# Kernel tuning notes

Hardware: AMD Instinct MI355X
Metric: run time of the kernel (lower is better)

Reference implementation:

```python
import jax, jax.numpy as jnp
import numpy as np

N, E, CIN, A, C, NB, B = 20000, 100000, 64, 32, 256, 4, 128
FD = C * NB  # fusion_dims = channels + c_growth*(n_blocks_out-1) with c_growth==channels
HID = 1024


def setup_inputs() -> dict:
    key = jax.random.key(0)
    ks = jax.random.split(key, 24)
    s = 0.05
    inp = {
        "x": jax.random.normal(ks[0], (N, CIN), jnp.float32),
        "edges": jax.random.randint(ks[1], (2, E), 0, N, jnp.int32),
        "edge_weights": jax.random.uniform(ks[2], (E,), jnp.float32),
        "edge_attrs": jax.random.normal(ks[3], (E, A), jnp.float32),
        "bbox_idx": jax.random.randint(ks[4], (N,), 0, B, jnp.int32),
        "num_boxes": B,
        # head GraphConv params: message MLP on [x_dst, x_src-x_dst, edge_attr]
        "W_msg0": jax.random.normal(ks[5], (2 * CIN + A, C), jnp.float32) * s,
        "b_msg0": jnp.zeros((C,), jnp.float32),
        "W_sup0": jax.random.normal(ks[6], (C + CIN, C), jnp.float32) * s,
        "b_sup0": jnp.zeros((C,), jnp.float32),
        # ResBlock params (n_blocks-1 blocks)
        "W_msg": jax.random.normal(ks[7], (NB - 1, 2 * C + A, C), jnp.float32) * s,
        "b_msg": jnp.zeros((NB - 1, C), jnp.float32),
        "W_sup": jax.random.normal(ks[8], (NB - 1, 2 * C, C), jnp.float32) * s,
        "b_sup": jnp.zeros((NB - 1, C), jnp.float32),
        # fusion MLPs [fusion_dims -> 1024]
        "W_fuse": jax.random.normal(ks[9], (FD, HID), jnp.float32) * s,
        "b_fuse": jnp.zeros((HID,), jnp.float32),
        "W_fuse_sup": jax.random.normal(ks[10], (FD, HID), jnp.float32) * s,
        "b_fuse_sup": jnp.zeros((HID,), jnp.float32),
    }
    return inp


def reference(x, edge_weights, edge_attrs, W_msg0, b_msg0, W_sup0, b_sup0,
              W_msg, b_msg, W_sup, b_sup, W_fuse, b_fuse, W_fuse_sup, b_fuse_sup,
              edges, bbox_idx, num_boxes):
    src, dst = edges[0], edges[1]
    n = x.shape[0]

    def gconv(f_in, Wm, bm):
        # per-edge message on [f_dst, f_src - f_dst, edge_attr], weighted sum-aggregate to dst
        h = jnp.concatenate([f_in[dst], f_in[src] - f_in[dst], edge_attrs], axis=1)
        m = jax.nn.relu(h @ Wm + bm) * edge_weights[:, None]
        return jax.ops.segment_sum(m, dst, num_segments=n)

    def super_node(f, x_node, Ws, bs):
        return jax.nn.relu(jnp.concatenate([f, x_node], axis=1) @ Ws + bs)

    # head GraphConv
    f = gconv(x, W_msg0, b_msg0)
    fs = super_node(f, x, W_sup0, b_sup0)
    feats, feats_super = [f], [fs]
    # ResBlocks: residual on node features, fresh super features
    for i in range(NB - 1):
        f = gconv(feats[-1], W_msg[i], b_msg[i]) + feats[-1]
        fs = super_node(f, feats_super[-1], W_sup[i], b_sup[i])
        feats.append(f)
        feats_super.append(fs)

    # n_blocks_out == n_blocks -> take all blocks
    feats_cat = jnp.concatenate(feats, axis=1)            # [N, FD]
    fusion = jax.nn.relu(feats_cat @ W_fuse + b_fuse)     # [N, 1024]
    out_feat = jnp.concatenate([fusion, feats_cat], axis=1)

    fs_cat = jnp.concatenate(feats_super, axis=1)         # [N, FD]
    sums = jax.ops.segment_sum(fs_cat, bbox_idx, num_segments=num_boxes)
    cnts = jax.ops.segment_sum(jnp.ones((n, 1), fs_cat.dtype), bbox_idx, num_segments=num_boxes)
    fs_mean = sums / jnp.maximum(cnts, 1.0)               # scatter(reduce='mean')
    fusion_sup = jax.nn.relu(fs_mean @ W_fuse_sup + b_fuse_sup)
    out_feat_super = jnp.concatenate([fusion_sup, fs_mean], axis=1)
    return out_feat, out_feat_super
```

## Files before the change

### kernel.cpp

```cpp
#include <hip/hip_runtime.h>

#define N_NODES 20000
#define N_EDGES 100000
#define CIN     64
#define A_DIM   32
#define CCH     256
#define NBOX    128
#define FD      1024
#define HID     1024
#define OUT_STRIDE 2048

typedef __attribute__((ext_vector_type(8))) short          short8;
typedef __attribute__((ext_vector_type(8))) unsigned short ushort8;
typedef __attribute__((ext_vector_type(4))) unsigned short ushort4v;
typedef __attribute__((ext_vector_type(4))) float          floatx4;

__device__ __forceinline__ unsigned short f2bf(float f) {
    unsigned int u = __float_as_uint(f);
    u += 0x7fff + ((u >> 16) & 1);
    return (unsigned short)(u >> 16);
}
__device__ __forceinline__ float bf2f(unsigned short h) {
    return __uint_as_float(((unsigned int)h) << 16);
}

__device__ __forceinline__ void glds16(const unsigned short* g, unsigned short* l) {
    __builtin_amdgcn_global_load_lds(
        (const __attribute__((address_space(1))) unsigned int*)g,
        (__attribute__((address_space(3))) unsigned int*)l,
        16, 0, 0);
}

struct GD {
    const unsigned short* src0b;
    const unsigned short* src1b;
    const unsigned short* Wt;
    const float* bias;
    const int* ridx0;
    float* outf;
    unsigned short* outb;
    int s0, o0, C0, s1, o1, do_relu, sof, oof, sob, oob, rmode, M, K, nbc;
};

__global__ __launch_bounds__(256) void mfma_dense(GD A, GD B, int n0)
{
    __shared__ __align__(16) unsigned short SM[2][4096];

    const int tid = threadIdx.x;
    const bool fa = (int)blockIdx.x < n0;

    const unsigned short* src0b = fa ? A.src0b : B.src0b;
    const unsigned short* src1b = fa ? A.src1b : B.src1b;
    const unsigned short* Wt    = fa ? A.Wt    : B.Wt;
    const float* bias           = fa ? A.bias  : B.bias;
    const int*   ridx0          = fa ? A.ridx0 : B.ridx0;
    float* outf                 = fa ? A.outf  : B.outf;
    unsigned short* outb        = fa ? A.outb  : B.outb;
    const int s0  = fa ? A.s0  : B.s0,  o0  = fa ? A.o0  : B.o0;
    const int C0  = fa ? A.C0  : B.C0;
    const int s1  = fa ? A.s1  : B.s1,  o1  = fa ? A.o1  : B.o1;
    const int do_relu = fa ? A.do_relu : B.do_relu;
    const int sof = fa ? A.sof : B.sof, oof = fa ? A.oof : B.oof;
    const int sob = fa ? A.sob : B.sob, oob = fa ? A.oob : B.oob;
    const int rmode = fa ? A.rmode : B.rmode;
    const int M   = fa ? A.M   : B.M;
    const int K   = fa ? A.K   : B.K;
    const int nbc = fa ? A.nbc : B.nbc;

    const int nwg = fa ? n0 : (int)gridDim.x - n0;
    const int lb  = (int)blockIdx.x - (fa ? 0 : n0);
    const int q8  = nwg >> 3, r8 = nwg & 7;
    const int xcd = lb & 7, boff = lb >> 3;
    const int bid = (xcd < r8 ? xcd * (q8 + 1)
                              : r8 * (q8 + 1) + (xcd - r8) * q8) + boff;

    const int rb   = bid / nbc, cb = bid % nbc;
    const int r0   = rb * 128, c0 = cb * 128;
    const int wave = tid >> 6, lane = tid & 63;
    const int quad = lane >> 4, l16 = lane & 15;
    const int wm   = (wave & 1) * 64, wn = (wave >> 1) * 64;

    int arow[2], grow[2], brow[2], kch[2];
    #pragma unroll
    for (int i = 0; i < 2; ++i) {
        const int g  = i * 256 + tid;
        const int rr = g >> 2;
        kch[i] = (g & 3) << 3;
        int gr2 = r0 + rr;
        if (gr2 >= M) gr2 = M - 1;
        grow[i] = gr2;
        arow[i] = ridx0 ? ridx0[gr2] : gr2;
        brow[i] = c0 + rr;
    }
    unsigned short* AsW = &SM[0][wave * 512];
    unsigned short* BsW = &SM[1][wave * 512];

    floatx4 acc[4][4];
    #pragma unroll
    for (int i = 0; i < 4; ++i)
        #pragma unroll
        for (int j = 0; j < 4; ++j) acc[i][j] = (floatx4){0.f, 0.f, 0.f, 0.f};

    for (int k0 = 0; k0 < K; k0 += 32) {
        #pragma unroll
        for (int i = 0; i < 2; ++i) {
            const int kk = k0 + kch[i];
            const unsigned short* ga = (kk < C0)
                ? src0b + (long)arow[i] * s0 + o0 + kk
                : src1b + (long)grow[i] * s1 + o1 + (kk - C0);
            glds16(ga, AsW + i * 2048);
            glds16(Wt + (long)brow[i] * K + k0 + kch[i], BsW + i * 2048);
        }
        __syncthreads();

        short8 af[4], bfr[4];
        #pragma unroll
        for (int mt = 0; mt < 4; ++mt)
            af[mt] = *(const short8*)(&SM[0][(wm + mt * 16 + l16) * 32 + quad * 8]);
        #pragma unroll
        for (int nt = 0; nt < 4; ++nt)
            bfr[nt] = *(const short8*)(&SM[1][(wn + nt * 16 + l16) * 32 + quad * 8]);
        #pragma unroll
        for (int mt = 0; mt < 4; ++mt)
            #pragma unroll
            for (int nt = 0; nt < 4; ++nt)
                acc[mt][nt] = __builtin_amdgcn_mfma_f32_16x16x32_bf16(
                    af[mt], bfr[nt], acc[mt][nt], 0, 0, 0);
        __syncthreads();
    }

    if (outf) {
        #pragma unroll
        for (int nt = 0; nt < 4; ++nt) {
            const int gc = c0 + wn + nt * 16 + l16;
            const float bv = bias ? bias[gc] : 0.f;
            #pragma unroll
            for (int mt = 0; mt < 4; ++mt) {
                #pragma unroll
                for (int reg = 0; reg < 4; ++reg) {
                    const int grr = r0 + wm + mt * 16 + quad * 4 + reg;
                    if (grr < M) {
                        float v = acc[mt][nt][reg] + bv;
                        if (do_relu) v = fmaxf(v, 0.f);
                        outf[(long)grr * sof + oof + gc] = v;
                    }
                }
            }
        }
    }
    if (outb) {
        unsigned short* Cs = &SM[0][0];
        #pragma unroll
        for (int p = 0; p < 2; ++p) {
            if (wm == p * 64) {
                #pragma unroll
                for (int nt = 0; nt < 4; ++nt) {
                    const int col = wn + nt * 16 + l16;
                    const float bv = bias ? bias[c0 + col] : 0.f;
                    #pragma unroll
                    for (int mt = 0; mt < 4; ++mt) {
                        #pragma unroll
                        for (int reg = 0; reg < 4; ++reg) {
                            float v = acc[mt][nt][reg] + bv;
                            if (do_relu) v = fmaxf(v, 0.f);
                            Cs[(mt * 16 + quad * 4 + reg) * 128 + col] = f2bf(v);
                        }
                    }
                }
            }
            __syncthreads();
            const int rl  = tid >> 2;
            const int cc0 = (tid & 3) << 3;
            const int grr2 = r0 + p * 64 + rl;
            if (grr2 < M) {
                const long rowbase = (rmode == 2)
                    ? ((long)(c0 >> 8) * ((long)N_EDGES * 256)
                       + (long)grr2 * 256 + (c0 & 255))
                    : ((long)grr2 * sob + oob + c0);
                #pragma unroll
                for (int j = 0; j < 4; ++j)
                    *(ushort8*)(outb + rowbase + cc0 + j * 32) =
                        *(const ushort8*)(&Cs[rl * 128 + cc0 + j * 32]);
            }
            __syncthreads();
        }
    }
}

__global__ __launch_bounds__(256) void agg_kernel(
    const unsigned short* __restrict__ pq,
    const int* __restrict__ rowptr,
    const int* __restrict__ ssrc,
    const float* __restrict__ sew,
    const unsigned short* __restrict__ Rb,
    const float* __restrict__ resid,
    const float* __restrict__ bias,
    float* __restrict__ out, int fofs, int rofs,
    unsigned short* __restrict__ nfbf, int nofs)
{
    const int wid  = (blockIdx.x * blockDim.x + threadIdx.x) >> 6;
    const int lane = threadIdx.x & 63;
    if (wid >= N_NODES) return;
    const int c = lane * 4;

    const ushort4v p4 = *(const ushort4v*)(pq + (long)wid * 512 + c);
    const float4 bb = *(const float4*)(bias + c);
    float pb[4] = {bf2f(p4[0]) + bb.x, bf2f(p4[1]) + bb.y,
                   bf2f(p4[2]) + bb.z, bf2f(p4[3]) + bb.w};
    float acc[4] = {0.f, 0.f, 0.f, 0.f};

    int s = rowptr[wid];
    const int sEnd = rowptr[wid + 1];

    ushort4v q4n, r4n;
    float wn_ = 0.f;
    if (s < sEnd) {
        const int srcn = ssrc[s];
        wn_ = sew[s];
        q4n = *(const ushort4v*)(pq + (long)srcn * 512 + 256 + c);
        r4n = *(const ushort4v*)(Rb + (long)s * 256 + c);
    }
    while (s < sEnd) {
        const ushort4v q4 = q4n, r4 = r4n;
        const float wgt = wn_;
        ++s;
        if (s < sEnd) {
            const int srcn = ssrc[s];
            wn_ = sew[s];
            q4n = *(const ushort4v*)(pq + (long)srcn * 512 + 256 + c);
            r4n = *(const ushort4v*)(Rb + (long)s * 256 + c);
        }
        #pragma unroll
        for (int j = 0; j < 4; ++j)
            acc[j] += fmaxf(pb[j] + bf2f(q4[j]) + bf2f(r4[j]), 0.f) * wgt;
    }
    if (rofs >= 0) {
        const float4 f4 = *(const float4*)(resid + (long)wid * OUT_STRIDE + rofs + c);
        acc[0] += f4.x; acc[1] += f4.y; acc[2] += f4.z; acc[3] += f4.w;
    }
    float4 o; o.x = acc[0]; o.y = acc[1]; o.z = acc[2]; o.w = acc[3];
    *(float4*)(out + (long)wid * OUT_STRIDE + fofs + c) = o;
    ushort4v hb = (ushort4v){f2bf(acc[0]), f2bf(acc[1]), f2bf(acc[2]), f2bf(acc[3])};
    *(ushort4v*)(nfbf + (long)wid * FD + nofs + c) = hb;
}

__device__ __forceinline__ void tr_block(const float* inp, unsigned short* outp,
                                         int K, int N, int bidx, int tid,
                                         float (*tile)[33])
{
    const int nbx = N >> 5;
    const int n0 = (bidx % nbx) << 5;
    const int k0 = (bidx / nbx) << 5;
    const int tx = tid & 31, ty = tid >> 5;
    #pragma unroll
    for (int r = 0; r < 4; ++r)
        tile[ty + r * 8][tx] = inp[(long)(k0 + ty + r * 8) * N + n0 + tx];
    __syncthreads();
    #pragma unroll
    for (int r = 0; r < 4; ++r)
        outp[(long)(n0 + ty + r * 8) * K + k0 + tx] = f2bf(tile[tx][ty + r * 8]);
}

#define PB_CVTX  1250
#define PB_CVTE  3125
#define PB_WPQ0  128
#define PB_WPQ3  384
#define PB_WTR   128
#define PB_TS0   80
#define PB_TS3   384
#define PB_TF    1024
#define PREP_BLOCKS (PB_CVTX+PB_CVTE+PB_WPQ0+PB_WPQ3+PB_WTR+PB_TS0+PB_TS3+PB_TF+PB_TF)

__global__ __launch_bounds__(256) void prep_all(
    const float* __restrict__ x, const float* __restrict__ ea,
    const float* __restrict__ W_msg0, const float* __restrict__ W_msg,
    const float* __restrict__ W_sup0, const float* __restrict__ W_sup,
    const float* __restrict__ W_fuse, const float* __restrict__ W_fsup,
    unsigned short* __restrict__ xb, unsigned short* __restrict__ eab,
    unsigned short* __restrict__ wpq0, unsigned short* __restrict__ wpq,
    unsigned short* __restrict__ wtr,
    unsigned short* __restrict__ wt_sup0, unsigned short* __restrict__ wt_sup,
    unsigned short* __restrict__ wt_fuse, unsigned short* __restrict__ wt_fsup)
{
    __shared__ float tile[32][33];
    const int tid = threadIdx.x;
    int b = blockIdx.x;

    if (b < PB_CVTX) {
        int i = b * 256 + tid;
        float4 v = ((const float4*)x)[i];
        ((ushort4v*)xb)[i] = (ushort4v){f2bf(v.x), f2bf(v.y), f2bf(v.z), f2bf(v.w)};
        return;
    }
    b -= PB_CVTX;
    if (b < PB_CVTE) {
        int i = b * 256 + tid;
        float4 v = ((const float4*)ea)[i];
        ((ushort4v*)eab)[i] = (ushort4v){f2bf(v.x), f2bf(v.y), f2bf(v.z), f2bf(v.w)};
        return;
    }
    b -= PB_CVTE;
    if (b < PB_WPQ0) {
        int i = b * 256 + tid;
        int nn = i >> 6, k = i & 63;
        float v = (nn < 256) ? (W_msg0[k * 256 + nn] - W_msg0[(64 + k) * 256 + nn])
                             : (W_msg0[(64 + k) * 256 + (nn - 256)]);
        wpq0[(long)nn * 64 + k] = f2bf(v);
        return;
    }
    b -= PB_WPQ0;
    if (b < PB_WPQ3) {
        const int slab = b / 128, bb = b % 128;
        const float* Wi = W_msg + (long)slab * 544 * 256;
        unsigned short* Wo = wpq + (long)slab * 512 * 256;
        const int n0 = (bb & 15) << 5;
        const int k0 = (bb >> 4) << 5;
        const int tx = tid & 31, ty = tid >> 5;
        #pragma unroll
        for (int r = 0; r < 4; ++r) {
            const int k = k0 + ty + r * 8;
            float v;
            if (n0 < 256)
                v = Wi[(long)k * 256 + n0 + tx] - Wi[(long)(256 + k) * 256 + n0 + tx];
            else
                v = Wi[(long)(256 + k) * 256 + (n0 - 256) + tx];
            tile[ty + r * 8][tx] = v;
        }
        __syncthreads();
        #pragma unroll
        for (int r = 0; r < 4; ++r)
            Wo[(long)(n0 + ty + r * 8) * 256 + k0 + tx] = f2bf(tile[tx][ty + r * 8]);
        return;
    }
    b -= PB_WPQ3;
    if (b < PB_WTR) {
        const int j = b >> 5;
        const float* Wi = (j == 0) ? (W_msg0 + 2 * CIN * 256)
                                   : (W_msg + (long)(j - 1) * 544 * 256 + 2 * CCH * 256);
        unsigned short* Wo = wtr + (long)j * 256 * 32;
        int i = (b & 31) * 256 + tid;
        int k = i >> 8, n = i & 255;
        Wo[(long)n * 32 + k] = f2bf(Wi[i]);
        return;
    }
    b -= PB_WTR;
    if (b < PB_TS0) { tr_block(W_sup0, wt_sup0, 320, 256, b, tid, tile); return; }
    b -= PB_TS0;
    if (b < PB_TS3) {
        const int slab = b / 128;
        tr_block(W_sup + (long)slab * 512 * 256, wt_sup + (long)slab * 256 * 512,
                 512, 256, b % 128, tid, tile);
        return;
    }
    b -= PB_TS3;
    if (b < PB_TF) { tr_block(W_fuse, wt_fuse, 1024, 1024, b, tid, tile); return; }
    b -= PB_TF;
    tr_block(W_fsup, wt_fsup, 1024, 1024, b, tid, tile);
}

__global__ void zero2(int* __restrict__ cnt, int* __restrict__ bcnt) {
    int i = blockIdx.x * blockDim.x + threadIdx.x;
    if (i < N_NODES + 1) cnt[i] = 0;
    else if (i - (N_NODES + 1) < 129) bcnt[i - (N_NODES + 1)] = 0;
}
__global__ void hist2(const int* __restrict__ dst, const int* __restrict__ bbox,
                      int* __restrict__ cnt, int* __restrict__ bcnt) {
    int i = blockIdx.x * blockDim.x + threadIdx.x;
    if (i < N_EDGES) atomicAdd(&cnt[dst[i]], 1);
    else if (i - N_EDGES < N_NODES) atomicAdd(&bcnt[bbox[i - N_EDGES]], 1);
}
__global__ __launch_bounds__(1024) void scan2(
    const int* __restrict__ cnt,  int* __restrict__ rowptr, int* __restrict__ ofs,
    const int* __restrict__ bcnt, int* __restrict__ bptr,   int* __restrict__ bofs)
{
    __shared__ int part[1024];
    const int tid = threadIdx.x;
    const int n = blockIdx.x == 0 ? N_NODES : NBOX;
    const int* c   = blockIdx.x == 0 ? cnt    : bcnt;
    int* rp        = blockIdx.x == 0 ? rowptr : bptr;
    int* op        = blockIdx.x == 0 ? ofs    : bofs;
    const int chunk = (n + 1023) >> 10;
    int s = 0;
    for (int j = 0; j < chunk; ++j) {
        int i = tid * chunk + j;
        if (i < n) s += c[i];
    }
    part[tid] = s; __syncthreads();
    for (int d = 1; d < 1024; d <<= 1) {
        int v = (tid >= d) ? part[tid - d] : 0;
        __syncthreads();
        part[tid] += v;
        __syncthreads();
    }
    int run = (tid > 0) ? part[tid - 1] : 0;
    for (int j = 0; j < chunk; ++j) {
        int i = tid * chunk + j;
        if (i < n) { rp[i] = run; op[i] = run; run += c[i]; }
    }
    if (tid == 1023) rp[n] = part[1023];
}
__global__ void scatter2(const int* __restrict__ src, const int* __restrict__ dst,
                         const float* __restrict__ ew, int* __restrict__ ofs,
                         int* __restrict__ ssrc, float* __restrict__ sew,
                         int* __restrict__ seid,
                         const int* __restrict__ bbox, int* __restrict__ bofs,
                         int* __restrict__ snode) {
    int i = blockIdx.x * blockDim.x + threadIdx.x;
    if (i < N_EDGES) {
        int pos = atomicAdd(&ofs[dst[i]], 1);
        ssrc[pos] = src[i];
        sew[pos]  = ew[i];
        seid[pos] = i;
    } else if (i - N_EDGES < N_NODES) {
        int j = i - N_EDGES;
        int pos = atomicAdd(&bofs[bbox[j]], 1);
        snode[pos] = j;
    }
}

__global__ __launch_bounds__(256) void box_mean_csr(
    const unsigned short* __restrict__ fsbf, const int* __restrict__ bptr,
    const int* __restrict__ snode, float* __restrict__ out_super,
    unsigned short* __restrict__ fsmeanb)
{
    const int b = blockIdx.x >> 2;
    const int c = ((blockIdx.x & 3) << 8) + threadIdx.x;
    const int s0 = bptr[b], s1 = bptr[b + 1];
    float sum = 0.f;
    for (int s = s0; s < s1; ++s)
        sum += bf2f(fsbf[(long)snode[s] * FD + c]);
    const float mean = sum / fmaxf((float)(s1 - s0), 1.f);
    out_super[(long)b * OUT_STRIDE + HID + c] = mean;
    fsmeanb[(long)b * FD + c] = f2bf(mean);
}

extern "C" void kernel_launch(void* const* d_in, const int* in_sizes, int n_in,
                              void* d_out, int out_size, void* d_ws, size_t ws_size,
                              hipStream_t stream) {
    const float* x      = (const float*)d_in[0];
    const int*   edges  = (const int*)d_in[1];
    const float* ew     = (const float*)d_in[2];
    const float* ea     = (const float*)d_in[3];
    const int*   bbox   = (const int*)d_in[4];
    const float* W_msg0 = (const float*)d_in[6];
    const float* b_msg0 = (const float*)d_in[7];
    const float* W_sup0 = (const float*)d_in[8];
    const float* b_sup0 = (const float*)d_in[9];
    const float* W_msg  = (const float*)d_in[10];
    const float* b_msg  = (const float*)d_in[11];
    const float* W_sup  = (const float*)d_in[12];
    const float* b_sup  = (const float*)d_in[13];
    const float* W_fuse = (const float*)d_in[14];
    const float* b_fuse = (const float*)d_in[15];
    const float* W_fsup = (const float*)d_in[16];
    const float* b_fsup = (const float*)d_in[17];

    float* out       = (float*)d_out;
    float* out_super = out + (long)N_NODES * OUT_STRIDE;

    char* w = (char*)d_ws;
    auto alloc = [&](size_t bytes) { char* p = w; w += (bytes + 63) & ~63ULL; return p; };
    unsigned short* fsbf    = (unsigned short*)alloc((size_t)N_NODES * FD * 2);
    unsigned short* nfbf    = (unsigned short*)alloc((size_t)N_NODES * FD * 2);
    unsigned short* pq      = (unsigned short*)alloc((size_t)N_NODES * 512 * 2);
    unsigned short* xb      = (unsigned short*)alloc((size_t)N_NODES * CIN * 2);
    unsigned short* eab     = (unsigned short*)alloc((size_t)N_EDGES * A_DIM * 2);
    unsigned short* Rb4     = (unsigned short*)alloc((size_t)N_EDGES * 1024 * 2);
    unsigned short* wpq0    = (unsigned short*)alloc((size_t)512 * CIN * 2);
    unsigned short* wpq     = (unsigned short*)alloc((size_t)3 * 512 * CCH * 2);
    unsigned short* wtr     = (unsigned short*)alloc((size_t)4 * 256 * 32 * 2);
    unsigned short* wt_sup0 = (unsigned short*)alloc((size_t)256 * 320 * 2);
    unsigned short* wt_sup  = (unsigned short*)alloc((size_t)3 * 256 * 512 * 2);
    unsigned short* wt_fuse = (unsigned short*)alloc((size_t)1024 * 1024 * 2);
    unsigned short* wt_fsup = (unsigned short*)alloc((size_t)1024 * 1024 * 2);
    unsigned short* fsmeanb = (unsigned short*)alloc((size_t)NBOX * FD * 2);
    float* sew        = (float*)alloc((size_t)N_EDGES * 4);
    int* cnt          = (int*)alloc((size_t)(N_NODES + 1) * 4);
    int* rowptr       = (int*)alloc((size_t)(N_NODES + 1) * 4);
    int* ofs          = (int*)alloc((size_t)(N_NODES + 1) * 4);
    int* ssrc         = (int*)alloc((size_t)N_EDGES * 4);
    int* seid         = (int*)alloc((size_t)N_EDGES * 4);
    int* bcnt         = (int*)alloc(129 * 4);
    int* bptr         = (int*)alloc(129 * 4);
    int* bofs         = (int*)alloc(129 * 4);
    int* snode        = (int*)alloc((size_t)N_NODES * 4);

    const int* srcp = edges;
    const int* dstp = edges + N_EDGES;

    prep_all<<<PREP_BLOCKS, 256, 0, stream>>>(
        x, ea, W_msg0, W_msg, W_sup0, W_sup, W_fuse, W_fsup,
        xb, eab, wpq0, wpq, wtr, wt_sup0, wt_sup, wt_fuse, wt_fsup);

    zero2<<<(N_NODES + 130 + 255) / 256, 256, 0, stream>>>(cnt, bcnt);
    hist2<<<(N_EDGES + N_NODES + 255) / 256, 256, 0, stream>>>(dstp, bbox, cnt, bcnt);
    scan2<<<2, 1024, 0, stream>>>(cnt, rowptr, ofs, bcnt, bptr, bofs);
    scatter2<<<(N_EDGES + N_NODES + 255) / 256, 256, 0, stream>>>(
        srcp, dstp, ew, ofs, ssrc, sew, seid, bbox, bofs, snode);

    const int GRB = (N_NODES + 127) / 128;
    const int GEB = (N_EDGES + 127) / 128;
    const long RLS = (long)N_EDGES * 256;

    auto mk = [](const unsigned short* src0b, int s0, int o0, int C0,
                 const int* ridx0,
                 const unsigned short* src1b, int s1, int o1,
                 const unsigned short* Wt, const float* bias, int relu,
                 float* outf, int sof, int oof,
                 unsigned short* outb, int sob, int oob, int rmode,
                 int M, int K, int nbc) {
        GD g;
        g.src0b = src0b; g.s0 = s0; g.o0 = o0; g.C0 = C0;
        g.ridx0 = ridx0;
        g.src1b = src1b; g.s1 = s1; g.o1 = o1;
        g.Wt = Wt; g.bias = bias; g.do_relu = relu;
        g.outf = outf; g.sof = sof; g.oof = oof;
        g.outb = outb; g.sob = sob; g.oob = oob; g.rmode = rmode;
        g.M = M; g.K = K; g.nbc = nbc;
        return g;
    };

    GD gR   = mk(eab, A_DIM, 0, A_DIM, seid, nullptr, 0, 0, wtr, nullptr, 0,
                 nullptr, 0, 0, Rb4, 0, 0, 2, N_EDGES, A_DIM, 8);
    GD gPQh = mk(xb, CIN, 0, CIN, nullptr, nullptr, 0, 0, wpq0, nullptr, 0,
                 nullptr, 0, 0, pq, 512, 0, 0, N_NODES, CIN, 4);
    GD gS0  = mk(nfbf, FD, 0, CCH, nullptr, xb, CIN, 0, wt_sup0, b_sup0, 1,
                 nullptr, 0, 0, fsbf, FD, 0, 0, N_NODES, CCH + CIN, 2);
    GD gPQ[3], gS[3];
    for (int i = 0; i < 3; ++i) {
        gPQ[i] = mk(nfbf, FD, CCH * i, CCH, nullptr, nullptr, 0, 0,
                    wpq + (long)i * 512 * CCH, nullptr, 0,
                    nullptr, 0, 0, pq, 512, 0, 0, N_NODES, CCH, 4);
        gS[i]  = mk(nfbf, FD, CCH * (i + 1), CCH, nullptr, fsbf, FD, CCH * i,
                    wt_sup + (long)i * 256 * 512, b_sup + i * CCH, 1,
                    nullptr, 0, 0, fsbf, FD, CCH * (i + 1), 0, N_NODES, 2 * CCH, 2);
    }
    GD gFU  = mk(nfbf, FD, 0, FD, nullptr, nullptr, 0, 0, wt_fuse, b_fuse, 1,
                 out, OUT_STRIDE, 0, nullptr, 0, 0, 0, N_NODES, FD, 8);
    GD gFS  = mk(fsmeanb, FD, 0, FD, nullptr, nullptr, 0, 0, wt_fsup, b_fsup, 1,
                 out_super, OUT_STRIDE, 0, nullptr, 0, 0, 0, NBOX, FD, 8);

    const int AGRID = (N_NODES + 3) / 4;

    mfma_dense<<<GEB * 8 + GRB * 4, 256, 0, stream>>>(gR, gPQh, GEB * 8);

    agg_kernel<<<AGRID, 256, 0, stream>>>(pq, rowptr, ssrc, sew,
        Rb4, out, b_msg0, out, HID, -1, nfbf, 0);

    mfma_dense<<<GRB * 6, 256, 0, stream>>>(gS0, gPQ[0], GRB * 2);
    for (int i = 0; i < 3; ++i) {
        agg_kernel<<<AGRID, 256, 0, stream>>>(pq, rowptr, ssrc, sew,
            Rb4 + (long)(i + 1) * RLS, out, b_msg + i * CCH,
            out, HID + CCH * (i + 1), HID + CCH * i, nfbf, CCH * (i + 1));
        if (i < 2)
            mfma_dense<<<GRB * 6, 256, 0, stream>>>(gS[i], gPQ[i + 1], GRB * 2);
    }

    mfma_dense<<<GRB * 10, 256, 0, stream>>>(gS[2], gFU, GRB * 2);

    box_mean_csr<<<NBOX * 4, 256, 0, stream>>>(fsbf, bptr, snode, out_super, fsmeanb);
    mfma_dense<<<8, 256, 0, stream>>>(gFS, gFS, 8);
}
```

Baseline: 789.1 us.

## Widen MFMA GEMM tile to 128x256 per workgroup

Doubles the N-dimension tile of the bf16 MFMA dense kernel from 128 to 256 columns. Each wave now computes a 64x128 sub-tile with 32 accumulators, and the LDS layout, epilogue staging (padded stride 264) and grid sizes are rewritten to match. The aim is to halve A-operand reloads and raise MFMA work per LDS load. In exchange it uses more registers per thread, which lowers occupancy, and launches fewer workgroups for the smaller GEMMs.

```diff
diff --git a/kernel.cpp b/kernel.cpp
--- a/kernel.cpp
+++ b/kernel.cpp
@@ -44,7 +44,7 @@
 
 __global__ __launch_bounds__(256) void mfma_dense(GD A, GD B, int n0)
 {
-    __shared__ __align__(16) unsigned short SM[2][4096];
+    __shared__ __align__(16) unsigned short SM[12288];
 
     const int tid = threadIdx.x;
     const bool fa = (int)blockIdx.x < n0;
@@ -75,55 +75,63 @@
                               : r8 * (q8 + 1) + (xcd - r8) * q8) + boff;
 
     const int rb   = bid / nbc, cb = bid % nbc;
-    const int r0   = rb * 128, c0 = cb * 128;
+    const int r0   = rb * 128, c0 = cb * 256;
     const int wave = tid >> 6, lane = tid & 63;
     const int quad = lane >> 4, l16 = lane & 15;
-    const int wm   = (wave & 1) * 64, wn = (wave >> 1) * 64;
-
-    int arow[2], grow[2], brow[2], kch[2];
+    const int wm   = (wave & 1) * 64, wn = (wave >> 1) * 128;
+
+    int arow[2], grow[2], kchA[2];
     #pragma unroll
     for (int i = 0; i < 2; ++i) {
         const int g  = i * 256 + tid;
         const int rr = g >> 2;
-        kch[i] = (g & 3) << 3;
+        kchA[i] = (g & 3) << 3;
         int gr2 = r0 + rr;
         if (gr2 >= M) gr2 = M - 1;
         grow[i] = gr2;
         arow[i] = ridx0 ? ridx0[gr2] : gr2;
-        brow[i] = c0 + rr;
-    }
-    unsigned short* AsW = &SM[0][wave * 512];
-    unsigned short* BsW = &SM[1][wave * 512];
-
-    floatx4 acc[4][4];
+    }
+    int brow[4], kchB[4];
+    #pragma unroll
+    for (int i = 0; i < 4; ++i) {
+        const int g = i * 256 + tid;
+        kchB[i] = (g & 3) << 3;
+        brow[i] = c0 + (g >> 2);
+    }
+    unsigned short* AsW = &SM[wave * 512];
+    unsigned short* BsW = &SM[4096 + wave * 512];
+
+    floatx4 acc[4][8];
     #pragma unroll
     for (int i = 0; i < 4; ++i)
         #pragma unroll
-        for (int j = 0; j < 4; ++j) acc[i][j] = (floatx4){0.f, 0.f, 0.f, 0.f};
+        for (int j = 0; j < 8; ++j) acc[i][j] = (floatx4){0.f, 0.f, 0.f, 0.f};
 
     for (int k0 = 0; k0 < K; k0 += 32) {
         #pragma unroll
         for (int i = 0; i < 2; ++i) {
-            const int kk = k0 + kch[i];
+            const int kk = k0 + kchA[i];
             const unsigned short* ga = (kk < C0)
                 ? src0b + (long)arow[i] * s0 + o0 + kk
                 : src1b + (long)grow[i] * s1 + o1 + (kk - C0);
             glds16(ga, AsW + i * 2048);
-            glds16(Wt + (long)brow[i] * K + k0 + kch[i], BsW + i * 2048);
         }
+        #pragma unroll
+        for (int i = 0; i < 4; ++i)
+            glds16(Wt + (long)brow[i] * K + k0 + kchB[i], BsW + i * 2048);
         __syncthreads();
 
-        short8 af[4], bfr[4];
+        short8 af[4], bfr[8];
         #pragma unroll
         for (int mt = 0; mt < 4; ++mt)
-            af[mt] = *(const short8*)(&SM[0][(wm + mt * 16 + l16) * 32 + quad * 8]);
-        #pragma unroll
-        for (int nt = 0; nt < 4; ++nt)
-            bfr[nt] = *(const short8*)(&SM[1][(wn + nt * 16 + l16) * 32 + quad * 8]);
+            af[mt] = *(const short8*)(&SM[(wm + mt * 16 + l16) * 32 + quad * 8]);
+        #pragma unroll
+        for (int nt = 0; nt < 8; ++nt)
+            bfr[nt] = *(const short8*)(&SM[4096 + (wn + nt * 16 + l16) * 32 + quad * 8]);
         #pragma unroll
         for (int mt = 0; mt < 4; ++mt)
             #pragma unroll
-            for (int nt = 0; nt < 4; ++nt)
+            for (int nt = 0; nt < 8; ++nt)
                 acc[mt][nt] = __builtin_amdgcn_mfma_f32_16x16x32_bf16(
                     af[mt], bfr[nt], acc[mt][nt], 0, 0, 0);
         __syncthreads();
@@ -131,7 +139,7 @@
 
     if (outf) {
         #pragma unroll
-        for (int nt = 0; nt < 4; ++nt) {
+        for (int nt = 0; nt < 8; ++nt) {
             const int gc = c0 + wn + nt * 16 + l16;
             const float bv = bias ? bias[gc] : 0.f;
             #pragma unroll
@@ -149,38 +157,38 @@
         }
     }
     if (outb) {
-        unsigned short* Cs = &SM[0][0];
-        #pragma unroll
-        for (int p = 0; p < 2; ++p) {
-            if (wm == p * 64) {
+        unsigned short* Cs = SM;
+        #pragma unroll
+        for (int p = 0; p < 4; ++p) {
+            if ((wave & 1) == (p >> 1)) {
                 #pragma unroll
-                for (int nt = 0; nt < 4; ++nt) {
-                    const int col = wn + nt * 16 + l16;
-                    const float bv = bias ? bias[c0 + col] : 0.f;
+                for (int m2 = 0; m2 < 2; ++m2) {
+                    const int mt = (p & 1) * 2 + m2;
                     #pragma unroll
-                    for (int mt = 0; mt < 4; ++mt) {
+                    for (int nt = 0; nt < 8; ++nt) {
+                        const int col = wn + nt * 16 + l16;
+                        const float bv = bias ? bias[c0 + col] : 0.f;
                         #pragma unroll
                         for (int reg = 0; reg < 4; ++reg) {
                             float v = acc[mt][nt][reg] + bv;
                             if (do_relu) v = fmaxf(v, 0.f);
-                            Cs[(mt * 16 + quad * 4 + reg) * 128 + col] = f2bf(v);
+                            Cs[(m2 * 16 + quad * 4 + reg) * 264 + col] = f2bf(v);
                         }
                     }
                 }
             }
             __syncthreads();
-            const int rl  = tid >> 2;
-            const int cc0 = (tid & 3) << 3;
-            const int grr2 = r0 + p * 64 + rl;
+            const int rl  = tid >> 3;
+            const int cs0 = (tid & 7) << 3;
+            const int grr2 = r0 + p * 32 + rl;
             if (grr2 < M) {
                 const long rowbase = (rmode == 2)
-                    ? ((long)(c0 >> 8) * ((long)N_EDGES * 256)
-                       + (long)grr2 * 256 + (c0 & 255))
+                    ? ((long)(c0 >> 8) * ((long)N_EDGES * 256) + (long)grr2 * 256)
                     : ((long)grr2 * sob + oob + c0);
                 #pragma unroll
-                for (int j = 0; j < 4; ++j)
-                    *(ushort8*)(outb + rowbase + cc0 + j * 32) =
-                        *(const ushort8*)(&Cs[rl * 128 + cc0 + j * 32]);
+                for (int k = 0; k < 4; ++k)
+                    *(ushort8*)(outb + rowbase + cs0 + k * 64) =
+                        *(const ushort8*)(&Cs[rl * 264 + cs0 + k * 64]);
             }
             __syncthreads();
         }
@@ -521,43 +529,43 @@
     };
 
     GD gR   = mk(eab, A_DIM, 0, A_DIM, seid, nullptr, 0, 0, wtr, nullptr, 0,
-                 nullptr, 0, 0, Rb4, 0, 0, 2, N_EDGES, A_DIM, 8);
+                 nullptr, 0, 0, Rb4, 0, 0, 2, N_EDGES, A_DIM, 4);
     GD gPQh = mk(xb, CIN, 0, CIN, nullptr, nullptr, 0, 0, wpq0, nullptr, 0,
-                 nullptr, 0, 0, pq, 512, 0, 0, N_NODES, CIN, 4);
+                 nullptr, 0, 0, pq, 512, 0, 0, N_NODES, CIN, 2);
     GD gS0  = mk(nfbf, FD, 0, CCH, nullptr, xb, CIN, 0, wt_sup0, b_sup0, 1,
-                 nullptr, 0, 0, fsbf, FD, 0, 0, N_NODES, CCH + CIN, 2);
+                 nullptr, 0, 0, fsbf, FD, 0, 0, N_NODES, CCH + CIN, 1);
     GD gPQ[3], gS[3];
     for (int i = 0; i < 3; ++i) {
         gPQ[i] = mk(nfbf, FD, CCH * i, CCH, nullptr, nullptr, 0, 0,
                     wpq + (long)i * 512 * CCH, nullptr, 0,
-                    nullptr, 0, 0, pq, 512, 0, 0, N_NODES, CCH, 4);
+                    nullptr, 0, 0, pq, 512, 0, 0, N_NODES, CCH, 2);
         gS[i]  = mk(nfbf, FD, CCH * (i + 1), CCH, nullptr, fsbf, FD, CCH * i,
                     wt_sup + (long)i * 256 * 512, b_sup + i * CCH, 1,
-                    nullptr, 0, 0, fsbf, FD, CCH * (i + 1), 0, N_NODES, 2 * CCH, 2);
+                    nullptr, 0, 0, fsbf, FD, CCH * (i + 1), 0, N_NODES, 2 * CCH, 1);
     }
     GD gFU  = mk(nfbf, FD, 0, FD, nullptr, nullptr, 0, 0, wt_fuse, b_fuse, 1,
-                 out, OUT_STRIDE, 0, nullptr, 0, 0, 0, N_NODES, FD, 8);
+                 out, OUT_STRIDE, 0, nullptr, 0, 0, 0, N_NODES, FD, 4);
     GD gFS  = mk(fsmeanb, FD, 0, FD, nullptr, nullptr, 0, 0, wt_fsup, b_fsup, 1,
-                 out_super, OUT_STRIDE, 0, nullptr, 0, 0, 0, NBOX, FD, 8);
+                 out_super, OUT_STRIDE, 0, nullptr, 0, 0, 0, NBOX, FD, 4);
 
     const int AGRID = (N_NODES + 3) / 4;
 
-    mfma_dense<<<GEB * 8 + GRB * 4, 256, 0, stream>>>(gR, gPQh, GEB * 8);
+    mfma_dense<<<GEB * 4 + GRB * 2, 256, 0, stream>>>(gR, gPQh, GEB * 4);
 
     agg_kernel<<<AGRID, 256, 0, stream>>>(pq, rowptr, ssrc, sew,
         Rb4, out, b_msg0, out, HID, -1, nfbf, 0);
 
-    mfma_dense<<<GRB * 6, 256, 0, stream>>>(gS0, gPQ[0], GRB * 2);
+    mfma_dense<<<GRB * 3, 256, 0, stream>>>(gS0, gPQ[0], GRB);
     for (int i = 0; i < 3; ++i) {
         agg_kernel<<<AGRID, 256, 0, stream>>>(pq, rowptr, ssrc, sew,
             Rb4 + (long)(i + 1) * RLS, out, b_msg + i * CCH,
             out, HID + CCH * (i + 1), HID + CCH * i, nfbf, CCH * (i + 1));
         if (i < 2)
-            mfma_dense<<<GRB * 6, 256, 0, stream>>>(gS[i], gPQ[i + 1], GRB * 2);
-    }
-
-    mfma_dense<<<GRB * 10, 256, 0, stream>>>(gS[2], gFU, GRB * 2);
+            mfma_dense<<<GRB * 3, 256, 0, stream>>>(gS[i], gPQ[i + 1], GRB);
+    }
+
+    mfma_dense<<<GRB * 5, 256, 0, stream>>>(gS[2], gFU, GRB);
 
     box_mean_csr<<<NBOX * 4, 256, 0, stream>>>(fsbf, bptr, snode, out_super, fsmeanb);
-    mfma_dense<<<8, 256, 0, stream>>>(gFS, gFS, 8);
-}
+    mfma_dense<<<4, 256, 0, stream>>>(gFS, gFS, 4);
+}
```

Result: slower. 1.018 ms (+29.0%).
